# Performance work log

Hardware: AMD Instinct MI355X
Metric: run time of the kernel (lower is better)

## Reference

```python
import jax, jax.numpy as jnp
import numpy as np

OVERFLOW_MARGIN = 1e-08


def setup_inputs() -> dict:
    key = jax.random.key(0)
    k1, k2, k3 = jax.random.split(key, 3)
    N, D, OUT = 8192, 256, 128
    values = jax.random.normal(k1, (N, D), dtype=jnp.float32)
    # adjacency: positive dense weights, self-connected (add identity)
    adjacency = jax.random.uniform(k2, (N, N), dtype=jnp.float32) + jnp.eye(N, dtype=jnp.float32)
    W = jax.random.normal(k3, (D, OUT), dtype=jnp.float32) * (1.0 / np.sqrt(D))
    b = jnp.zeros((OUT,), dtype=jnp.float32)
    return {"values": values, "adjacency": adjacency, "W": W, "b": b}


def reference(values, adjacency, W, b):
    # fc_sc = Dense(values)
    fc = values @ W + b                                   # [N, OUT]
    # symmetric degree normalization: L = D^{-1/2} A D^{-1/2}
    d = jnp.sum(adjacency, axis=1, keepdims=True)         # [N, 1] == A @ ones
    d_inv_sqrt = (d + OVERFLOW_MARGIN) ** -0.5            # [N, 1]
    # L @ fc expressed as elementwise row/col scaling around one GEMM
    # (mathematically identical to diag(dinv) @ A @ diag(dinv) @ fc)
    out = d_inv_sqrt * (adjacency @ (d_inv_sqrt * fc))    # [N, OUT]
    return out
```

## Files before the change

kernel.cpp:

```cpp
#include <hip/hip_runtime.h>
#include <hip/hip_bf16.h>
#include <stdint.h>

#define N_NODES 8192
#define D_IN 256
#define D_OUT 128
#define BKK 64

typedef __bf16 bf16x8 __attribute__((ext_vector_type(8)));
typedef __bf16 bf16x4 __attribute__((ext_vector_type(4)));
typedef float f32x4 __attribute__((ext_vector_type(4)));

__global__ __launch_bounds__(256) void k_rowsum(const float* __restrict__ A,
                                                float* __restrict__ dinv) {
  const int r = blockIdx.x;
  const int t = threadIdx.x;
  const float4* row = (const float4*)(A + (size_t)r * N_NODES);
  float s = 0.f;
#pragma unroll
  for (int i = 0; i < 8; ++i) {
    float4 v = row[t + i * 256];
    s += (v.x + v.y) + (v.z + v.w);
  }
#pragma unroll
  for (int off = 32; off > 0; off >>= 1) s += __shfl_down(s, off, 64);
  __shared__ float wsum[4];
  if ((t & 63) == 0) wsum[t >> 6] = s;
  __syncthreads();
  if (t == 0) {
    float d = ((wsum[0] + wsum[1]) + (wsum[2] + wsum[3])) + 1e-8f;
    dinv[r] = 1.0f / sqrtf(d);
  }
}

__global__ __launch_bounds__(256) void k_fc(const float* __restrict__ values,
                                            const float* __restrict__ W,
                                            const float* __restrict__ bias,
                                            const float* __restrict__ dinv,
                                            __bf16* __restrict__ yT) {
  __shared__ float vsm[8 * 256];
  __shared__ float wsm[64 * 128];
  const int t = threadIdx.x;
  const int rb = blockIdx.x * 8;
  {
    const float4* src = (const float4*)(values + (size_t)rb * D_IN);
    float4* dst = (float4*)vsm;
    dst[t] = src[t];
    dst[t + 256] = src[t + 256];
  }
  const int c = t & 127;
  const int rh = t >> 7;
  float a0 = 0.f, a1 = 0.f, a2 = 0.f, a3 = 0.f;
  for (int kb = 0; kb < 4; ++kb) {
    __syncthreads();
    {
      const float4* src = (const float4*)(W + kb * 64 * D_OUT);
      float4* dst = (float4*)wsm;
#pragma unroll
      for (int i = 0; i < 8; ++i) dst[t + i * 256] = src[t + i * 256];
    }
    __syncthreads();
    const float* vrow = vsm + (rh * 4) * 256 + kb * 64;
#pragma unroll 8
    for (int k = 0; k < 64; ++k) {
      float wv = wsm[k * D_OUT + c];
      a0 = fmaf(vrow[k], wv, a0);
      a1 = fmaf(vrow[256 + k], wv, a1);
      a2 = fmaf(vrow[512 + k], wv, a2);
      a3 = fmaf(vrow[768 + k], wv, a3);
    }
  }
  const float bc = bias[c];
  const int rg = rb + rh * 4;
  bf16x4 p;
  p[0] = (__bf16)((a0 + bc) * dinv[rg + 0]);
  p[1] = (__bf16)((a1 + bc) * dinv[rg + 1]);
  p[2] = (__bf16)((a2 + bc) * dinv[rg + 2]);
  p[3] = (__bf16)((a3 + bc) * dinv[rg + 3]);
  *(bf16x4*)(yT + (size_t)c * N_NODES + rg) = p;
}

__device__ __forceinline__ void gload_lds16(const void* gp, void* lp) {
  __builtin_amdgcn_global_load_lds((const __attribute__((address_space(1))) void*)gp,
                                   (__attribute__((address_space(3))) void*)lp, 16, 0, 0);
}

__global__ __launch_bounds__(256) void k_gemm(const float* __restrict__ A,
                                              const __bf16* __restrict__ yT,
                                              const float* __restrict__ dinv,
                                              float* __restrict__ out) {
  __shared__ __align__(16) char smA[2][32 * 128];
  __shared__ __align__(16) char smB[2][128 * 128];
  const int t = threadIdx.x;
  const int l = t & 63;
  const int w = t >> 6;
  const int mb = blockIdx.x * 32;

  const int am = t >> 3;
  const int aseg = t & 7;
  const float* agp = A + (size_t)(mb + am) * N_NODES + aseg * 8;
  const int awr = am * 128 + ((aseg ^ (am & 7)) * 16);

  const int bn_base = w * 8 + (l >> 3);
  const int bseg = l & 7;

  f32x4 acc00 = {}, acc01 = {}, acc10 = {}, acc11 = {};

  const int lr = l & 15;
  const int lg = l >> 4;

  int aoff[2][2], boff[2][2];
#pragma unroll
  for (int mf = 0; mf < 2; ++mf)
#pragma unroll
    for (int ks = 0; ks < 2; ++ks) {
      int m = mf * 16 + lr;
      int seg = ks * 4 + lg;
      aoff[mf][ks] = m * 128 + ((seg ^ (m & 7)) * 16);
      int n = w * 32 + mf * 16 + lr;
      boff[mf][ks] = n * 128 + ((seg ^ (n & 7)) * 16);
    }

  auto stageB = [&](int kb, int buf) {
#pragma unroll
    for (int q = 0; q < 4; ++q) {
      int n = q * 32 + bn_base;
      const __bf16* gp = yT + (size_t)n * N_NODES + kb + ((bseg ^ (n & 7)) * 8);
      void* lp = (void*)(&smB[buf][0] + q * 4096 + w * 1024);
      gload_lds16(gp, lp);
    }
  };

  stageB(0, 0);
  {
    float4 v0 = *(const float4*)(agp + 0);
    float4 v1 = *(const float4*)(agp + 4);
    bf16x8 h;
    h[0] = (__bf16)v0.x; h[1] = (__bf16)v0.y; h[2] = (__bf16)v0.z; h[3] = (__bf16)v0.w;
    h[4] = (__bf16)v1.x; h[5] = (__bf16)v1.y; h[6] = (__bf16)v1.z; h[7] = (__bf16)v1.w;
    *(bf16x8*)(&smA[0][0] + awr) = h;
  }
  __syncthreads();

  int cur = 0;
  for (int step = 0; step < N_NODES / BKK; ++step) {
    const int nxt = cur ^ 1;
    const bool pf = (step + 1 < N_NODES / BKK);
    float4 v0, v1;
    if (pf) {
      stageB((step + 1) * BKK, nxt);
      v0 = *(const float4*)(agp + (step + 1) * BKK);
      v1 = *(const float4*)(agp + (step + 1) * BKK + 4);
    }
#pragma unroll
    for (int ks = 0; ks < 2; ++ks) {
      bf16x8 af0 = *(const bf16x8*)(&smA[cur][0] + aoff[0][ks]);
      bf16x8 af1 = *(const bf16x8*)(&smA[cur][0] + aoff[1][ks]);
      bf16x8 bf0 = *(const bf16x8*)(&smB[cur][0] + boff[0][ks]);
      bf16x8 bf1 = *(const bf16x8*)(&smB[cur][0] + boff[1][ks]);
      acc00 = __builtin_amdgcn_mfma_f32_16x16x32_bf16(af0, bf0, acc00, 0, 0, 0);
      acc01 = __builtin_amdgcn_mfma_f32_16x16x32_bf16(af0, bf1, acc01, 0, 0, 0);
      acc10 = __builtin_amdgcn_mfma_f32_16x16x32_bf16(af1, bf0, acc10, 0, 0, 0);
      acc11 = __builtin_amdgcn_mfma_f32_16x16x32_bf16(af1, bf1, acc11, 0, 0, 0);
    }
    if (pf) {
      bf16x8 h;
      h[0] = (__bf16)v0.x; h[1] = (__bf16)v0.y; h[2] = (__bf16)v0.z; h[3] = (__bf16)v0.w;
      h[4] = (__bf16)v1.x; h[5] = (__bf16)v1.y; h[6] = (__bf16)v1.z; h[7] = (__bf16)v1.w;
      *(bf16x8*)(&smA[nxt][0] + awr) = h;
    }
    __syncthreads();
    cur = nxt;
  }

#pragma unroll
  for (int mf = 0; mf < 2; ++mf) {
#pragma unroll
    for (int nf = 0; nf < 2; ++nf) {
      f32x4 a = (mf == 0) ? ((nf == 0) ? acc00 : acc01) : ((nf == 0) ? acc10 : acc11);
      const int col = w * 32 + nf * 16 + lr;
      const int rowb = mb + mf * 16 + lg * 4;
#pragma unroll
      for (int v2 = 0; v2 < 4; ++v2) {
        const int r = rowb + v2;
        out[(size_t)r * D_OUT + col] = dinv[r] * a[v2];
      }
    }
  }
}

extern "C" void kernel_launch(void* const* d_in, const int* in_sizes, int n_in,
                              void* d_out, int out_size, void* d_ws, size_t ws_size,
                              hipStream_t stream) {
  const float* values = (const float*)d_in[0];
  const float* A = (const float*)d_in[1];
  const float* W = (const float*)d_in[2];
  const float* bias = (const float*)d_in[3];
  float* out = (float*)d_out;

  float* dinv = (float*)d_ws;
  __bf16* yT = (__bf16*)((char*)d_ws + 32768);

  k_rowsum<<<N_NODES, 256, 0, stream>>>(A, dinv);
  k_fc<<<N_NODES / 8, 256, 0, stream>>>(values, W, bias, dinv, yT);
  k_gemm<<<N_NODES / 32, 256, 0, stream>>>(A, yT, dinv, out);
}
```

Measured before the change: 524.6 us.

## Pre-convert adjacency to bf16 in rowsum pass, split-K GEMM, register-tiled fc

The row-sum kernel now also writes a bf16 copy of the adjacency matrix, so the main GEMM streams half the bytes and can load A straight into LDS with async global_load_lds instead of converting it in registers. The GEMM is split along K into two halves to double the number of blocks, and a new finish kernel adds the two partial sums and applies the row scaling. The fc kernel is rewritten with 4x4 register tiles per thread that read W directly from global memory. The trade-off is an extra 128MB bf16 write plus a reread of that copy, along with partial-buffer traffic and one more launch.

After: 456.2 us. -13.0%, faster.

```diff
diff --git a/kernel.cpp b/kernel.cpp
--- a/kernel.cpp
+++ b/kernel.cpp
@@ -6,21 +6,27 @@
 #define D_IN 256
 #define D_OUT 128
 #define BKK 64
+#define KSPLIT 2
 
 typedef __bf16 bf16x8 __attribute__((ext_vector_type(8)));
 typedef __bf16 bf16x4 __attribute__((ext_vector_type(4)));
 typedef float f32x4 __attribute__((ext_vector_type(4)));
 
-__global__ __launch_bounds__(256) void k_rowsum(const float* __restrict__ A,
-                                                float* __restrict__ dinv) {
+__global__ __launch_bounds__(256) void k_prep(const float* __restrict__ A,
+                                              __bf16* __restrict__ Abf,
+                                              float* __restrict__ dinv) {
   const int r = blockIdx.x;
   const int t = threadIdx.x;
-  const float4* row = (const float4*)(A + (size_t)r * N_NODES);
+  const f32x4* row = (const f32x4*)(A + (size_t)r * N_NODES);
+  bf16x4* orow = (bf16x4*)(Abf + (size_t)r * N_NODES);
   float s = 0.f;
 #pragma unroll
   for (int i = 0; i < 8; ++i) {
-    float4 v = row[t + i * 256];
-    s += (v.x + v.y) + (v.z + v.w);
+    f32x4 v = __builtin_nontemporal_load(&row[t + i * 256]);
+    s += (v[0] + v[1]) + (v[2] + v[3]);
+    bf16x4 h;
+    h[0] = (__bf16)v[0]; h[1] = (__bf16)v[1]; h[2] = (__bf16)v[2]; h[3] = (__bf16)v[3];
+    orow[t + i * 256] = h;
   }
 #pragma unroll
   for (int off = 32; off > 0; off >>= 1) s += __shfl_down(s, off, 64);
@@ -33,51 +39,58 @@
   }
 }
 
+#define VPAD 260
 __global__ __launch_bounds__(256) void k_fc(const float* __restrict__ values,
                                             const float* __restrict__ W,
                                             const float* __restrict__ bias,
                                             const float* __restrict__ dinv,
                                             __bf16* __restrict__ yT) {
-  __shared__ float vsm[8 * 256];
-  __shared__ float wsm[64 * 128];
+  __shared__ float vsm[32 * VPAD];
   const int t = threadIdx.x;
-  const int rb = blockIdx.x * 8;
+  const int rb = blockIdx.x * 32;
   {
     const float4* src = (const float4*)(values + (size_t)rb * D_IN);
-    float4* dst = (float4*)vsm;
-    dst[t] = src[t];
-    dst[t + 256] = src[t + 256];
-  }
-  const int c = t & 127;
-  const int rh = t >> 7;
-  float a0 = 0.f, a1 = 0.f, a2 = 0.f, a3 = 0.f;
-  for (int kb = 0; kb < 4; ++kb) {
-    __syncthreads();
-    {
-      const float4* src = (const float4*)(W + kb * 64 * D_OUT);
-      float4* dst = (float4*)wsm;
-#pragma unroll
-      for (int i = 0; i < 8; ++i) dst[t + i * 256] = src[t + i * 256];
-    }
-    __syncthreads();
-    const float* vrow = vsm + (rh * 4) * 256 + kb * 64;
-#pragma unroll 8
-    for (int k = 0; k < 64; ++k) {
-      float wv = wsm[k * D_OUT + c];
-      a0 = fmaf(vrow[k], wv, a0);
-      a1 = fmaf(vrow[256 + k], wv, a1);
-      a2 = fmaf(vrow[512 + k], wv, a2);
-      a3 = fmaf(vrow[768 + k], wv, a3);
-    }
-  }
-  const float bc = bias[c];
-  const int rg = rb + rh * 4;
-  bf16x4 p;
-  p[0] = (__bf16)((a0 + bc) * dinv[rg + 0]);
-  p[1] = (__bf16)((a1 + bc) * dinv[rg + 1]);
-  p[2] = (__bf16)((a2 + bc) * dinv[rg + 2]);
-  p[3] = (__bf16)((a3 + bc) * dinv[rg + 3]);
-  *(bf16x4*)(yT + (size_t)c * N_NODES + rg) = p;
+#pragma unroll
+    for (int i = 0; i < 8; ++i) {
+      int f = t + i * 256;
+      int r = f >> 6, kq = f & 63;
+      *(float4*)(vsm + r * VPAD + kq * 4) = src[f];
+    }
+  }
+  __syncthreads();
+  const int tr = t >> 5, tc = t & 31;
+  const int c0 = tc * 4;
+  float accm[4][4] = {};
+  const float* vr = vsm + (tr * 4) * VPAD;
+#pragma unroll 4
+  for (int k4 = 0; k4 < 64; ++k4) {
+    f32x4 a[4];
+    float4 wv[4];
+#pragma unroll
+    for (int i = 0; i < 4; ++i) a[i] = *(const f32x4*)(vr + i * VPAD + k4 * 4);
+#pragma unroll
+    for (int kk = 0; kk < 4; ++kk) wv[kk] = *(const float4*)(W + (size_t)(k4 * 4 + kk) * D_OUT + c0);
+#pragma unroll
+    for (int i = 0; i < 4; ++i) {
+      accm[i][0] += a[i][0] * wv[0].x + a[i][1] * wv[1].x + a[i][2] * wv[2].x + a[i][3] * wv[3].x;
+      accm[i][1] += a[i][0] * wv[0].y + a[i][1] * wv[1].y + a[i][2] * wv[2].y + a[i][3] * wv[3].y;
+      accm[i][2] += a[i][0] * wv[0].z + a[i][1] * wv[1].z + a[i][2] * wv[2].z + a[i][3] * wv[3].z;
+      accm[i][3] += a[i][0] * wv[0].w + a[i][1] * wv[1].w + a[i][2] * wv[2].w + a[i][3] * wv[3].w;
+    }
+  }
+  const int rg = rb + tr * 4;
+  float dv[4];
+#pragma unroll
+  for (int i = 0; i < 4; ++i) dv[i] = dinv[rg + i];
+#pragma unroll
+  for (int j = 0; j < 4; ++j) {
+    const int c = c0 + j;
+    const float bc = bias[c];
+    bf16x4 p;
+#pragma unroll
+    for (int i = 0; i < 4; ++i) p[i] = (__bf16)((accm[i][j] + bc) * dv[i]);
+    *(bf16x4*)(yT + (size_t)c * N_NODES + rg) = p;
+  }
 }
 
 __device__ __forceinline__ void gload_lds16(const void* gp, void* lp) {
@@ -85,27 +98,24 @@
                                    (__attribute__((address_space(3))) void*)lp, 16, 0, 0);
 }
 
-__global__ __launch_bounds__(256) void k_gemm(const float* __restrict__ A,
+__global__ __launch_bounds__(256) void k_gemm(const __bf16* __restrict__ Abf,
                                               const __bf16* __restrict__ yT,
-                                              const float* __restrict__ dinv,
-                                              float* __restrict__ out) {
+                                              float* __restrict__ partial) {
   __shared__ __align__(16) char smA[2][32 * 128];
   __shared__ __align__(16) char smB[2][128 * 128];
   const int t = threadIdx.x;
   const int l = t & 63;
   const int w = t >> 6;
   const int mb = blockIdx.x * 32;
-
-  const int am = t >> 3;
-  const int aseg = t & 7;
-  const float* agp = A + (size_t)(mb + am) * N_NODES + aseg * 8;
-  const int awr = am * 128 + ((aseg ^ (am & 7)) * 16);
-
+  const int k0 = blockIdx.y * (N_NODES / KSPLIT);
+  float* pout = partial + (size_t)blockIdx.y * N_NODES * D_OUT;
+
+  const int am = t >> 3, aseg = t & 7;
+  const __bf16* agp = Abf + (size_t)(mb + am) * N_NODES + k0 + ((aseg ^ (am & 7)) * 8);
   const int bn_base = w * 8 + (l >> 3);
   const int bseg = l & 7;
 
   f32x4 acc00 = {}, acc01 = {}, acc10 = {}, acc11 = {};
-
   const int lr = l & 15;
   const int lg = l >> 4;
 
@@ -121,53 +131,34 @@
       boff[mf][ks] = n * 128 + ((seg ^ (n & 7)) * 16);
     }
 
-  auto stageB = [&](int kb, int buf) {
+  auto stage = [&](int kb, int buf) {
+    gload_lds16(agp + kb, (void*)(&smA[buf][0] + w * 1024));
 #pragma unroll
     for (int q = 0; q < 4; ++q) {
       int n = q * 32 + bn_base;
-      const __bf16* gp = yT + (size_t)n * N_NODES + kb + ((bseg ^ (n & 7)) * 8);
-      void* lp = (void*)(&smB[buf][0] + q * 4096 + w * 1024);
-      gload_lds16(gp, lp);
+      const __bf16* gp = yT + (size_t)n * N_NODES + k0 + kb + ((bseg ^ (n & 7)) * 8);
+      gload_lds16(gp, (void*)(&smB[buf][0] + q * 4096 + w * 1024));
     }
   };
 
-  stageB(0, 0);
-  {
-    float4 v0 = *(const float4*)(agp + 0);
-    float4 v1 = *(const float4*)(agp + 4);
-    bf16x8 h;
-    h[0] = (__bf16)v0.x; h[1] = (__bf16)v0.y; h[2] = (__bf16)v0.z; h[3] = (__bf16)v0.w;
-    h[4] = (__bf16)v1.x; h[5] = (__bf16)v1.y; h[6] = (__bf16)v1.z; h[7] = (__bf16)v1.w;
-    *(bf16x8*)(&smA[0][0] + awr) = h;
-  }
+  stage(0, 0);
   __syncthreads();
 
+  const int KSTEPS = (N_NODES / KSPLIT) / BKK;
   int cur = 0;
-  for (int step = 0; step < N_NODES / BKK; ++step) {
+  for (int step = 0; step < KSTEPS; ++step) {
     const int nxt = cur ^ 1;
-    const bool pf = (step + 1 < N_NODES / BKK);
-    float4 v0, v1;
-    if (pf) {
-      stageB((step + 1) * BKK, nxt);
-      v0 = *(const float4*)(agp + (step + 1) * BKK);
-      v1 = *(const float4*)(agp + (step + 1) * BKK + 4);
-    }
+    if (step + 1 < KSTEPS) stage((step + 1) * BKK, nxt);
 #pragma unroll
     for (int ks = 0; ks < 2; ++ks) {
       bf16x8 af0 = *(const bf16x8*)(&smA[cur][0] + aoff[0][ks]);
       bf16x8 af1 = *(const bf16x8*)(&smA[cur][0] + aoff[1][ks]);
-      bf16x8 bf0 = *(const bf16x8*)(&smB[cur][0] + boff[0][ks]);
-      bf16x8 bf1 = *(const bf16x8*)(&smB[cur][0] + boff[1][ks]);
-      acc00 = __builtin_amdgcn_mfma_f32_16x16x32_bf16(af0, bf0, acc00, 0, 0, 0);
-      acc01 = __builtin_amdgcn_mfma_f32_16x16x32_bf16(af0, bf1, acc01, 0, 0, 0);
-      acc10 = __builtin_amdgcn_mfma_f32_16x16x32_bf16(af1, bf0, acc10, 0, 0, 0);
-      acc11 = __builtin_amdgcn_mfma_f32_16x16x32_bf16(af1, bf1, acc11, 0, 0, 0);
-    }
-    if (pf) {
-      bf16x8 h;
-      h[0] = (__bf16)v0.x; h[1] = (__bf16)v0.y; h[2] = (__bf16)v0.z; h[3] = (__bf16)v0.w;
-      h[4] = (__bf16)v1.x; h[5] = (__bf16)v1.y; h[6] = (__bf16)v1.z; h[7] = (__bf16)v1.w;
-      *(bf16x8*)(&smA[nxt][0] + awr) = h;
+      bf16x8 bq0 = *(const bf16x8*)(&smB[cur][0] + boff[0][ks]);
+      bf16x8 bq1 = *(const bf16x8*)(&smB[cur][0] + boff[1][ks]);
+      acc00 = __builtin_amdgcn_mfma_f32_16x16x32_bf16(af0, bq0, acc00, 0, 0, 0);
+      acc01 = __builtin_amdgcn_mfma_f32_16x16x32_bf16(af0, bq1, acc01, 0, 0, 0);
+      acc10 = __builtin_amdgcn_mfma_f32_16x16x32_bf16(af1, bq0, acc10, 0, 0, 0);
+      acc11 = __builtin_amdgcn_mfma_f32_16x16x32_bf16(af1, bq1, acc11, 0, 0, 0);
     }
     __syncthreads();
     cur = nxt;
@@ -182,11 +173,22 @@
       const int rowb = mb + mf * 16 + lg * 4;
 #pragma unroll
       for (int v2 = 0; v2 < 4; ++v2) {
-        const int r = rowb + v2;
-        out[(size_t)r * D_OUT + col] = dinv[r] * a[v2];
+        pout[(size_t)(rowb + v2) * D_OUT + col] = a[v2];
       }
     }
   }
+}
+
+__global__ __launch_bounds__(256) void k_finish(const float* __restrict__ partial,
+                                                const float* __restrict__ dinv,
+                                                float* __restrict__ out) {
+  const int i = blockIdx.x * 256 + threadIdx.x;
+  const f32x4* p0 = (const f32x4*)partial;
+  const f32x4* p1 = (const f32x4*)(partial + (size_t)N_NODES * D_OUT);
+  f32x4 a = p0[i] + p1[i];
+  const float dv = dinv[i >> 5];
+  f32x4* o = (f32x4*)out;
+  o[i] = a * dv;
 }
 
 extern "C" void kernel_launch(void* const* d_in, const int* in_sizes, int n_in,
@@ -198,10 +200,14 @@
   const float* bias = (const float*)d_in[3];
   float* out = (float*)d_out;
 
-  float* dinv = (float*)d_ws;
-  __bf16* yT = (__bf16*)((char*)d_ws + 32768);
-
-  k_rowsum<<<N_NODES, 256, 0, stream>>>(A, dinv);
-  k_fc<<<N_NODES / 8, 256, 0, stream>>>(values, W, bias, dinv, yT);
-  k_gemm<<<N_NODES / 32, 256, 0, stream>>>(A, yT, dinv, out);
-}
+  char* ws = (char*)d_ws;
+  float* dinv = (float*)ws;
+  __bf16* yT = (__bf16*)(ws + (64 << 10));
+  float* partial = (float*)(ws + (4 << 20));
+  __bf16* Abf = (__bf16*)(ws + (16 << 20));
+
+  k_prep<<<N_NODES, 256, 0, stream>>>(A, Abf, dinv);
+  k_fc<<<N_NODES / 32, 256, 0, stream>>>(values, W, bias, dinv, yT);
+  k_gemm<<<dim3(N_NODES / 32, KSPLIT), 256, 0, stream>>>(Abf, yT, partial);
+  k_finish<<<N_NODES * D_OUT / 4 / 256, 256, 0, stream>>>(partial, dinv, out);
+}
```
